# Optimization experiments

Hardware: AMD Instinct MI355X
Metric: run time of the kernel (lower is better)

Reference implementation:

```python
import jax, jax.numpy as jnp
import numpy as np

B, L, D_MODEL, H, DK = 4, 1024, 1024, 16, 64
FILTER_LENGTHS = (2, 4)
FMAX = max(FILTER_LENGTHS)


def setup_inputs() -> dict:
    key = jax.random.key(0)
    ks = jax.random.split(key, 12)
    s = 0.02
    inp = {
        "Q": jax.random.normal(ks[0], (B, L, D_MODEL), jnp.float32),
        "K": jax.random.normal(ks[1], (B, L, D_MODEL), jnp.float32),
        "V": jax.random.normal(ks[2], (B, L, D_MODEL), jnp.float32),
        "attn_mask": jnp.zeros((1,), jnp.bool_),
        "WQ": jax.random.normal(ks[3], (D_MODEL, H * DK), jnp.float32) * s,
        "bQ": jnp.zeros((H * DK,), jnp.float32),
        "WK": jax.random.normal(ks[4], (D_MODEL, H * DK), jnp.float32) * s,
        "bK": jnp.zeros((H * DK,), jnp.float32),
        "WV": jax.random.normal(ks[5], (D_MODEL, H * DK), jnp.float32) * s,
        "bV": jnp.zeros((H * DK,), jnp.float32),
        "Wfc": jax.random.normal(ks[6], (H * DK, D_MODEL), jnp.float32) * s,
        "bfc": jnp.zeros((D_MODEL,), jnp.float32),
        "conv_q": jax.random.normal(ks[7], (H * DK, H * DK, FMAX), jnp.float32) * s,
        "conv_k": jax.random.normal(ks[8], (H * DK, H * DK, FMAX), jnp.float32) * s,
        "w": jax.random.normal(ks[9], (len(FILTER_LENGTHS),), jnp.float32),
    }
    return inp


def _get_conv(x4, conv, w):
    # x4: (b, h, l, d_k) -> ACAT.get_conv with torch-identical raw reshapes
    b, h, l, d_k = x4.shape
    sig = x4.reshape(b, h * d_k, l)            # raw row-major reshape (as torch)
    pad = jnp.pad(sig, ((0, 0), (0, 0), (FMAX // 2, FMAX // 2)))
    idx = jnp.arange(l)[:, None] + jnp.arange(FMAX)[None, :]   # (l, FMAX) unfold windows
    seq = pad[:, :, idx]                        # (b, d, l, FMAX)
    f_s = jnp.array(FILTER_LENGTHS, dtype=sig.dtype)
    w_f = f_s * w                               # einsum('f,f->f')
    ind = jnp.argmax(w_f)
    flen = jnp.array(FILTER_LENGTHS)[ind]
    mask = (jnp.arange(FMAX) < flen).astype(sig.dtype)
    seq = seq * mask                            # zero out trailing taps
    out = jnp.einsum('bdlf,dof->blo', seq, conv)  # o = h*d_k
    return out.reshape(b, h, l, d_k)            # raw reshape as in torch code


def reference(Q, K, V, attn_mask, WQ, bQ, WK, bK, WV, bV, Wfc, bfc, conv_q, conv_k, w):
    b, l, _ = Q.shape
    q = (Q @ WQ + bQ).reshape(b, l, H, DK).transpose(0, 2, 1, 3)  # (b,h,l,dk)
    k = (K @ WK + bK).reshape(b, l, H, DK).transpose(0, 2, 1, 3)
    v = (V @ WV + bV).reshape(b, l, H, DK).transpose(0, 2, 1, 3)
    q = _get_conv(q, conv_q, w) + q
    k = _get_conv(k, conv_k, w) + k
    scores = jnp.einsum('bhqd,bhkd->bhqk', q, k) / np.sqrt(DK).astype(np.float32)
    attn = jax.nn.softmax(scores, axis=-1)
    ctx = jnp.einsum('bhqk,bhkd->bhqd', attn, v)
    ctx = ctx.transpose(0, 2, 1, 3).reshape(b, l, H * DK)
    out = ctx @ Wfc + bfc
    return out
```

## Files before the change

### kernel.cpp

```cpp
#include <hip/hip_runtime.h>
#include <hip/hip_bf16.h>

typedef _Float16 f16;
typedef _Float16 f16x2 __attribute__((ext_vector_type(2)));
typedef _Float16 f16x4 __attribute__((ext_vector_type(4)));
typedef _Float16 f16x8 __attribute__((ext_vector_type(8)));
typedef float f32x4 __attribute__((ext_vector_type(4)));

__device__ __forceinline__ f16x2 pkrtz(float a, float b) {
    auto r = __builtin_amdgcn_cvt_pkrtz(a, b);
    f16x2 o; o[0] = (f16)r[0]; o[1] = (f16)r[1];
    return o;
}

#define XT_ROWS 1027
#define XT_BSTRIDE (XT_ROWS * 1024)

__device__ __forceinline__ void gload16(const f16* g, f16* l) {
    __builtin_amdgcn_global_load_lds(
        (const __attribute__((address_space(1))) void*)g,
        (__attribute__((address_space(3))) void*)l, 16, 0, 0);
}

__device__ __forceinline__ void stage_tile(const f16* src, int ld, f16* lds)
{
    const int tid = threadIdx.x;
    const int w512 = (tid >> 6) << 9;
    #pragma unroll
    for (int q = 0; q < 4; ++q) {
        const int s = q * 256 + tid;
        const int row = s >> 3;
        const int col = ((s & 7) ^ (row & 7)) << 3;
        gload16(src + row * ld + col, lds + (q << 11) + w512);
    }
}

__device__ __forceinline__ void stage64(const f16* src, int ld, f16* lds)
{
    const int tid = threadIdx.x;
    const int w512 = (tid >> 6) << 9;
    #pragma unroll
    for (int q = 0; q < 2; ++q) {
        const int s = q * 256 + tid;
        const int row = s >> 3;
        const int col = ((s & 7) ^ (row & 7)) << 3;
        gload16(src + row * ld + col, lds + (q << 11) + w512);
    }
}

template <int CONV>
__device__ __forceinline__ void gemm_core64(
    const f16* __restrict__ A, int lda, int m0,
    const f16* __restrict__ Bt, int ldb, int K,
    f16* Alds, f16* Blds, f32x4 acc[4][4])
{
    const int tid = threadIdx.x;
    const int lid = tid & 63;
    const int wv  = tid >> 6;
    const int wm  = (wv >> 1) * 64;
    const int wn  = (wv & 1) * 64;
    const int g   = lid >> 4;
    const int r15 = lid & 15;

    stage_tile(A + m0 * lda, lda, Alds);
    stage_tile(Bt, ldb, Blds);
    asm volatile("s_waitcnt vmcnt(0)" ::: "memory");
    __builtin_amdgcn_s_barrier();

    for (int k0 = 0; k0 < K; k0 += 64) {
        f16x8 af[2][4], bf[2][4];
        #pragma unroll
        for (int kc = 0; kc < 2; ++kc) {
            #pragma unroll
            for (int mi = 0; mi < 4; ++mi) {
                const int row = wm + mi * 16 + r15;
                af[kc][mi] = *(const f16x8*)(Alds + row * 64 +
                                             (((kc * 4 + g) ^ (row & 7)) << 3));
            }
            #pragma unroll
            for (int nj = 0; nj < 4; ++nj) {
                const int row = wn + nj * 16 + r15;
                bf[kc][nj] = *(const f16x8*)(Blds + row * 64 +
                                             (((kc * 4 + g) ^ (row & 7)) << 3));
            }
        }
        asm volatile("s_waitcnt lgkmcnt(0)" ::: "memory");
        __builtin_amdgcn_sched_barrier(0);
        __builtin_amdgcn_s_barrier();
        const int k1 = k0 + 64;
        if (k1 < K) {
            const f16* Asrc;
            if (CONV) Asrc = A + (m0 + (k1 >> 10)) * lda + (k1 & 1023);
            else      Asrc = A + m0 * lda + k1;
            stage_tile(Asrc, lda, Alds);
            stage_tile(Bt + k1, ldb, Blds);
        }
        __builtin_amdgcn_sched_barrier(0);
        #pragma unroll
        for (int kc = 0; kc < 2; ++kc)
            #pragma unroll
            for (int mi = 0; mi < 4; ++mi)
                #pragma unroll
                for (int nj = 0; nj < 4; ++nj)
                    acc[mi][nj] = __builtin_amdgcn_mfma_f32_16x16x32_f16(
                        af[kc][mi], bf[kc][nj], acc[mi][nj], 0, 0, 0);
        __builtin_amdgcn_sched_barrier(0);
        asm volatile("s_waitcnt vmcnt(0)" ::: "memory");
        __builtin_amdgcn_s_barrier();
    }
}

__global__ __launch_bounds__(256) void k_cvt_all(
    const float* __restrict__ Q, const float* __restrict__ K,
    const float* __restrict__ V, f16* __restrict__ Qh,
    f16* __restrict__ Kh, f16* __restrict__ Vh)
{
    const int bid = blockIdx.x;
    const int which = bid >> 12;
    const int i = (bid & 4095) * 256 + threadIdx.x;
    const float* in = which == 0 ? Q : which == 1 ? K : V;
    f16* out = which == 0 ? Qh : which == 1 ? Kh : Vh;
    float4 v = ((const float4*)in)[i];
    f16x4 o;
    o[0] = (f16)v.x; o[1] = (f16)v.y; o[2] = (f16)v.z; o[3] = (f16)v.w;
    ((f16x4*)out)[i] = o;
}

__global__ __launch_bounds__(256) void k_wtrans(
    const float* __restrict__ WQ, const float* __restrict__ WK,
    const float* __restrict__ WV, const float* __restrict__ Wfc,
    f16* __restrict__ WQt, f16* __restrict__ WKt,
    f16* __restrict__ WVt, f16* __restrict__ WFt)
{
    const int z = blockIdx.z;
    const float* in = z == 0 ? WQ : z == 1 ? WK : z == 2 ? WV : Wfc;
    f16* out = z == 0 ? WQt : z == 1 ? WKt : z == 2 ? WVt : WFt;
    __shared__ float tile[32][33];
    int c0 = blockIdx.x * 32, r0 = blockIdx.y * 32;
    int tx = threadIdx.x, ty = threadIdx.y;
    #pragma unroll
    for (int i = ty; i < 32; i += 8)
        tile[i][tx] = in[(size_t)(r0 + i) * 1024 + c0 + tx];
    __syncthreads();
    #pragma unroll
    for (int i = ty; i < 32; i += 8)
        out[(size_t)(c0 + i) * 1024 + r0 + tx] = (f16)tile[tx][i];
}

__global__ __launch_bounds__(256) void k_ctrans(
    const float* __restrict__ convq, const float* __restrict__ convk,
    f16* __restrict__ CTq, f16* __restrict__ CTk)
{
    const float* in = blockIdx.z ? convk : convq;
    f16* out = blockIdx.z ? CTk : CTq;
    __shared__ float tile[32][33];
    int c0 = blockIdx.x * 32, r0 = blockIdx.y * 32;
    int tx = threadIdx.x, ty = threadIdx.y;
    #pragma unroll
    for (int i = ty; i < 32; i += 8)
        tile[i][tx] = in[(size_t)(r0 + i) * 4096 + c0 + tx];
    __syncthreads();
    #pragma unroll
    for (int i = ty; i < 32; i += 8)
        out[(size_t)(c0 + i) * 1024 + r0 + tx] = (f16)tile[tx][i];
}

__global__ __launch_bounds__(256) void k_transpose_pad(
    const f16* __restrict__ qx4, const f16* __restrict__ kx4,
    f16* __restrict__ XtQ, f16* __restrict__ XtK)
{
    int z = blockIdx.z, b = z & 3, ten = z >> 2;
    const f16* in = (ten ? kx4 : qx4) + (size_t)b * 1048576;
    f16* out = (ten ? XtK : XtQ) + (size_t)b * XT_BSTRIDE;
    __shared__ f16 tile[32][33];
    int c0 = blockIdx.x * 32;
    int tp0 = blockIdx.y * 32;
    int tx = threadIdx.x, ty = threadIdx.y;
    #pragma unroll
    for (int i = ty; i < 32; i += 8) {
        int t = tp0 + tx - 2;
        tile[i][tx] = (t >= 0 && t < 1024) ? in[(c0 + i) * 1024 + t] : (f16)0.f;
    }
    __syncthreads();
    #pragma unroll
    for (int i = ty; i < 32; i += 8) {
        int tp = tp0 + i;
        if (tp < XT_ROWS) out[tp * 1024 + c0 + tx] = tile[tx][i];
    }
}

__global__ __launch_bounds__(256) void k_gemm_proj(
    const f16* __restrict__ Qh, const f16* __restrict__ Kh, const f16* __restrict__ Vh,
    const f16* __restrict__ WQt, const f16* __restrict__ WKt, const f16* __restrict__ WVt,
    const float* __restrict__ bQ, const float* __restrict__ bK, const float* __restrict__ bV,
    f16* __restrict__ qx4, f16* __restrict__ kx4, f16* __restrict__ vT)
{
    __shared__ __align__(16) f16 Alds[128 * 64];
    __shared__ __align__(16) f16 Blds[128 * 64];
    const int nid = blockIdx.x + blockIdx.y * 8 + blockIdx.z * 256;
    const int wgid = (nid & 7) * 96 + (nid >> 3);
    const int xw = wgid & 7, yw = (wgid >> 3) & 31, z = wgid >> 8;
    const f16* A  = z == 0 ? Qh : z == 1 ? Kh : Vh;
    const f16* Bt = z == 0 ? WQt : z == 1 ? WKt : WVt;
    const float* bias = z == 0 ? bQ : z == 1 ? bK : bV;
    f16* dst = z == 0 ? qx4 : z == 1 ? kx4 : vT;
    const int m0 = yw * 128, n0 = xw * 128;
    f32x4 acc[4][4] = {};
    gemm_core64<0>(A, 1024, m0, Bt + n0 * 1024, 1024, 1024, Alds, Blds, acc);

    const int tid = threadIdx.x, lid = tid & 63, wv = tid >> 6;
    const int wm = (wv >> 1) * 64, wn = (wv & 1) * 64, g = lid >> 4, r15 = lid & 15;
    #pragma unroll
    for (int nj = 0; nj < 4; ++nj) {
        const int col = n0 + wn + nj * 16 + r15;
        const float bv = bias[col];
        const int h = col >> 6, d = col & 63;
        #pragma unroll
        for (int mi = 0; mi < 4; ++mi)
            #pragma unroll
            for (int j = 0; j < 4; ++j) {
                const int row = m0 + wm + mi * 16 + g * 4 + j;
                const int b = row >> 10, l = row & 1023;
                const float v = acc[mi][nj][j] + bv;
                const int off = b * 1048576 + h * 65536 +
                                (z == 2 ? (d * 1024 + l) : (l * 64 + d));
                dst[off] = (f16)v;
            }
    }
}

__global__ __launch_bounds__(256) void k_gemm_conv(
    const f16* __restrict__ XtQ, const f16* __restrict__ XtK,
    const f16* __restrict__ CTq, const f16* __restrict__ CTk,
    f16* __restrict__ qx4, f16* __restrict__ kx4,
    const float* __restrict__ wvec)
{
    __shared__ __align__(16) f16 Alds[128 * 64];
    __shared__ __align__(16) f16 Blds[128 * 64];
    const int nid = blockIdx.x + blockIdx.y * 8 + blockIdx.z * 64;
    const int z = nid & 7;
    const int inner = nid >> 3;
    const int yw = inner & 7;
    const int xw = inner >> 3;
    const int b = z & 3, ten = z >> 2;
    const f16* Xt = (ten ? XtK : XtQ) + (size_t)b * XT_BSTRIDE;
    const f16* CT = ten ? CTk : CTq;
    f16* dst = (ten ? kx4 : qx4) + (size_t)b * 1048576;

    const int flen = (2.f * wvec[0] >= 4.f * wvec[1]) ? 2 : 4;
    const int K = flen << 10;

    const int m0 = yw * 128, n0 = xw * 128;
    f32x4 acc[4][4] = {};
    gemm_core64<1>(Xt, 1024, m0, CT + n0 * 4096, 4096, K, Alds, Blds, acc);

    const int tid = threadIdx.x, lid = tid & 63, wv = tid >> 6;
    const int wm = (wv >> 1) * 64, wn = (wv & 1) * 64, g = lid >> 4, r15 = lid & 15;
    #pragma unroll
    for (int nj = 0; nj < 4; ++nj) {
        const int col = n0 + wn + nj * 16 + r15;
        #pragma unroll
        for (int mi = 0; mi < 4; ++mi)
            #pragma unroll
            for (int j = 0; j < 4; ++j) {
                const int row = m0 + wm + mi * 16 + g * 4 + j;
                const int i = row * 1024 + col;
                dst[i] = (f16)(acc[mi][nj][j] + (float)dst[i]);
            }
    }
}

__device__ __forceinline__ void attn_tile(
    const f16* KL, const f16* VL,
    const f16* Kn, const f16* Vn, f16* KLn, f16* VLn, bool doStage,
    const f16x8 qf[2][2], f32x4 o[2][4], f32x4 lsum[2], int g, int r15)
{
    f16x8 kf[4][2];
    #pragma unroll
    for (int nj = 0; nj < 4; ++nj)
        #pragma unroll
        for (int kc = 0; kc < 2; ++kc) {
            const int row = nj * 16 + r15;
            kf[nj][kc] = *(const f16x8*)(KL + row * 64 +
                                         (((kc * 4 + g) ^ (row & 7)) << 3));
        }
    f16x4 vlo[4][2], vhi[4][2];
    #pragma unroll
    for (int db = 0; db < 4; ++db)
        #pragma unroll
        for (int ch = 0; ch < 2; ++ch) {
            const int row = db * 16 + r15;
            const int c1 = ch * 4 + (g >> 1);
            const int c2 = c1 + 2;
            const int sub = (g & 1) * 4;
            vlo[db][ch] = *(const f16x4*)(VL + row * 64 +
                                          ((c1 ^ (row & 7)) << 3) + sub);
            vhi[db][ch] = *(const f16x4*)(VL + row * 64 +
                                          ((c2 ^ (row & 7)) << 3) + sub);
        }
    asm volatile("s_waitcnt lgkmcnt(0)" ::: "memory");
    __builtin_amdgcn_sched_barrier(0);
    __builtin_amdgcn_s_barrier();
    if (doStage) {
        stage64(Kn, 64, KLn);
        stage64(Vn, 1024, VLn);
    }
    __builtin_amdgcn_sched_barrier(0);
    f32x4 sacc[2][4] = {};
    #pragma unroll
    for (int nj = 0; nj < 4; ++nj)
        #pragma unroll
        for (int kc = 0; kc < 2; ++kc) {
            sacc[0][nj] = __builtin_amdgcn_mfma_f32_16x16x32_f16(
                kf[nj][kc], qf[0][kc], sacc[0][nj], 0, 0, 0);
            sacc[1][nj] = __builtin_amdgcn_mfma_f32_16x16x32_f16(
                kf[nj][kc], qf[1][kc], sacc[1][nj], 0, 0, 0);
        }
    #pragma unroll
    for (int qh = 0; qh < 2; ++qh) {
        f32x4 pe[4];
        #pragma unroll
        for (int nj = 0; nj < 4; ++nj) {
            #pragma unroll
            for (int j = 0; j < 4; ++j)
                pe[nj][j] = __expf(sacc[qh][nj][j] - 2.0f);
            lsum[qh] += pe[nj];
        }
        f16x8 pb[2];
        #pragma unroll
        for (int ch = 0; ch < 2; ++ch) {
            union { f16x2 h2[4]; f16x8 v8; } u;
            u.h2[0] = pkrtz(pe[2 * ch][0], pe[2 * ch][1]);
            u.h2[1] = pkrtz(pe[2 * ch][2], pe[2 * ch][3]);
            u.h2[2] = pkrtz(pe[2 * ch + 1][0], pe[2 * ch + 1][1]);
            u.h2[3] = pkrtz(pe[2 * ch + 1][2], pe[2 * ch + 1][3]);
            pb[ch] = u.v8;
        }
        #pragma unroll
        for (int db = 0; db < 4; ++db)
            #pragma unroll
            for (int ch = 0; ch < 2; ++ch) {
                union { f16x4 h4[2]; f16x8 v8; } w;
                w.h4[0] = vlo[db][ch];
                w.h4[1] = vhi[db][ch];
                o[qh][db] = __builtin_amdgcn_mfma_f32_16x16x32_f16(
                    w.v8, pb[ch], o[qh][db], 0, 0, 0);
            }
    }
    __builtin_amdgcn_sched_barrier(0);
    asm volatile("s_waitcnt vmcnt(0)" ::: "memory");
    __builtin_amdgcn_s_barrier();
}

__global__ __launch_bounds__(256) void k_attn(
    const f16* __restrict__ qn, const f16* __restrict__ kn,
    const f16* __restrict__ vT, f16* __restrict__ ctx)
{
    __shared__ __align__(16) f16 lds[4][4096];
    const int bh = blockIdx.x, b = bh >> 4, h = bh & 15;
    const f16* Qp = qn + (size_t)b * 1048576 + h * 65536;
    const f16* Kp = kn + (size_t)b * 1048576 + h * 65536;
    const f16* Vp = vT + (size_t)b * 1048576 + h * 65536;
    const int tid = threadIdx.x, lid = tid & 63, wv = tid >> 6;
    const int g = lid >> 4, r15 = lid & 15;
    const int q0 = blockIdx.y * 128 + wv * 32;

    f16x8 qf[2][2];
    #pragma unroll
    for (int qh = 0; qh < 2; ++qh)
        #pragma unroll
        for (int kc = 0; kc < 2; ++kc) {
            f16x8 t = *(const f16x8*)(Qp + (q0 + qh * 16 + r15) * 64 + kc * 32 + g * 8);
            #pragma unroll
            for (int e = 0; e < 8; ++e) t[e] = t[e] * (f16)0.125f;
            qf[qh][kc] = t;
        }

    f32x4 o[2][4] = {};
    f32x4 lsum[2] = {};

    stage64(Kp, 64, lds[0]);
    stage64(Vp, 1024, lds[1]);
    asm volatile("s_waitcnt vmcnt(0)" ::: "memory");
    __builtin_amdgcn_s_barrier();

    for (int tt = 0; tt < 8; ++tt) {
        const int t1 = 2 * tt + 1;
        attn_tile(lds[0], lds[1], Kp + t1 * 4096, Vp + t1 * 64,
                  lds[2], lds[3], true, qf, o, lsum, g, r15);
        attn_tile(lds[2], lds[3], Kp + (t1 + 1) * 4096, Vp + (t1 + 1) * 64,
                  lds[0], lds[1], tt < 7, qf, o, lsum, g, r15);
    }

    float inv[2];
    #pragma unroll
    for (int qh = 0; qh < 2; ++qh) {
        float lr = lsum[qh][0] + lsum[qh][1] + lsum[qh][2] + lsum[qh][3];
        lr += __shfl_xor(lr, 16);
        lr += __shfl_xor(lr, 32);
        inv[qh] = 1.0f / lr;
    }
    f16* Olds = &lds[0][0] + wv * (32 * 72);
    #pragma unroll
    for (int qh = 0; qh < 2; ++qh)
        #pragma unroll
        for (int db = 0; db < 4; ++db) {
            const int row = qh * 16 + r15, col = db * 16 + g * 4;
            *(f16x2*)(Olds + row * 72 + col) =
                pkrtz(o[qh][db][0] * inv[qh], o[qh][db][1] * inv[qh]);
            *(f16x2*)(Olds + row * 72 + col + 2) =
                pkrtz(o[qh][db][2] * inv[qh], o[qh][db][3] * inv[qh]);
        }
    asm volatile("s_waitcnt lgkmcnt(0)" ::: "memory");
    __builtin_amdgcn_sched_barrier(0);
    #pragma unroll
    for (int p = 0; p < 4; ++p) {
        const int row = p * 8 + (lid >> 3);
        const int c8 = (lid & 7) * 8;
        f16x8 v = *(const f16x8*)(Olds + row * 72 + c8);
        *(f16x8*)(ctx + (size_t)b * 1048576 + (q0 + row) * 1024 + h * 64 + c8) = v;
    }
}

__global__ __launch_bounds__(256) void k_gemm_final(
    const f16* __restrict__ ctx, const f16* __restrict__ WFt,
    const float* __restrict__ bfc, float* __restrict__ out)
{
    __shared__ __align__(16) f16 Alds[128 * 64];
    __shared__ __align__(16) f16 Blds[128 * 64];
    const int nid = blockIdx.x + blockIdx.y * 8;
    const int wgid = (nid & 7) * 32 + (nid >> 3);
    const int xw = wgid & 7, yw = wgid >> 3;
    const int m0 = yw * 128, n0 = xw * 128;
    f32x4 acc[4][4] = {};
    gemm_core64<0>(ctx, 1024, m0, WFt + n0 * 1024, 1024, 1024, Alds, Blds, acc);

    const int tid = threadIdx.x, lid = tid & 63, wv = tid >> 6;
    const int wm = (wv >> 1) * 64, wn = (wv & 1) * 64, g = lid >> 4, r15 = lid & 15;
    #pragma unroll
    for (int nj = 0; nj < 4; ++nj) {
        const int col = n0 + wn + nj * 16 + r15;
        const float bv = bfc[col];
        #pragma unroll
        for (int mi = 0; mi < 4; ++mi)
            #pragma unroll
            for (int j = 0; j < 4; ++j) {
                const int row = m0 + wm + mi * 16 + g * 4 + j;
                out[(size_t)row * 1024 + col] = acc[mi][nj][j] + bv;
            }
    }
}

extern "C" void kernel_launch(void* const* d_in, const int* in_sizes, int n_in,
                              void* d_out, int out_size, void* d_ws, size_t ws_size,
                              hipStream_t stream)
{
    (void)in_sizes; (void)n_in; (void)out_size; (void)ws_size;
    const float* Q     = (const float*)d_in[0];
    const float* K     = (const float*)d_in[1];
    const float* V     = (const float*)d_in[2];
    const float* WQ    = (const float*)d_in[4];
    const float* bQ    = (const float*)d_in[5];
    const float* WK    = (const float*)d_in[6];
    const float* bK    = (const float*)d_in[7];
    const float* WV    = (const float*)d_in[8];
    const float* bV    = (const float*)d_in[9];
    const float* Wfc   = (const float*)d_in[10];
    const float* bfc   = (const float*)d_in[11];
    const float* convq = (const float*)d_in[12];
    const float* convk = (const float*)d_in[13];
    const float* w     = (const float*)d_in[14];

    char* ws = (char*)d_ws;
    f16* qx4   = (f16*)(ws + 0);
    f16* kx4   = (f16*)(ws + 8388608);
    f16* vT    = (f16*)(ws + 16777216);
    f16* WFt   = (f16*)(ws + 25165824);
    f16* Qh    = (f16*)(ws + 27262976);
    f16* Kh    = (f16*)(ws + 35651584);
    f16* Vh    = (f16*)(ws + 44040192);
    f16* WQt   = (f16*)(ws + 52428800);
    f16* WKt   = (f16*)(ws + 54525952);
    f16* WVt   = (f16*)(ws + 56623104);
    f16* CTq   = (f16*)(ws + 58720256);
    f16* XtQ   = (f16*)(ws + 27262976);
    f16* XtK   = (f16*)(ws + 35676160);
    f16* CTk   = (f16*)(ws + 44089344);
    f16* ctxb  = (f16*)(ws + 27262976);

    dim3 b256(256), bT(32, 8);

    k_cvt_all<<<12288, b256, 0, stream>>>(Q, K, V, Qh, Kh, Vh);
    k_wtrans<<<dim3(32, 32, 4), bT, 0, stream>>>(WQ, WK, WV, Wfc,
                                                 WQt, WKt, WVt, WFt);
    k_gemm_proj<<<dim3(8, 32, 3), b256, 0, stream>>>(Qh, Kh, Vh, WQt, WKt, WVt,
                                                     bQ, bK, bV, qx4, kx4, vT);
    k_transpose_pad<<<dim3(32, 33, 8), bT, 0, stream>>>(qx4, kx4, XtQ, XtK);
    k_ctrans<<<dim3(128, 32, 2), bT, 0, stream>>>(convq, convk, CTq, CTk);
    k_gemm_conv<<<dim3(8, 8, 8), b256, 0, stream>>>(XtQ, XtK, CTq, CTk,
                                                    qx4, kx4, w);
    k_attn<<<dim3(64, 8), b256, 0, stream>>>(qx4, kx4, vT, ctxb);
    k_gemm_final<<<dim3(8, 32), b256, 0, stream>>>(ctxb, WFt, bfc, (float*)d_out);
}
```

Before: 182.3 us.

## Double-buffer LDS tiles in shared GEMM core to prefetch two stages ahead

Replaces the single-buffer GEMM main loop with a double-buffered one. The loop now prefetches the tile two k-steps ahead and waits with a partial vmcnt, so global loads overlap more of the MFMA work. LDS use per block doubles to 64 KB, which can reduce occupancy. The vmcnt(8) count assumes each stage issues exactly 8 loads, so correctness depends on the stage_tile load count.

```diff
diff --git a/kernel.cpp b/kernel.cpp
--- a/kernel.cpp
+++ b/kernel.cpp
@@ -49,10 +49,10 @@
 }
 
 template <int CONV>
-__device__ __forceinline__ void gemm_core64(
+__device__ __forceinline__ void gemm_core_db(
     const f16* __restrict__ A, int lda, int m0,
     const f16* __restrict__ Bt, int ldb, int K,
-    f16* Alds, f16* Blds, f32x4 acc[4][4])
+    f16* Alds0, f16* Blds0, f16* Alds1, f16* Blds1, f32x4 acc[4][4])
 {
     const int tid = threadIdx.x;
     const int lid = tid & 63;
@@ -62,38 +62,47 @@
     const int g   = lid >> 4;
     const int r15 = lid & 15;
 
-    stage_tile(A + m0 * lda, lda, Alds);
-    stage_tile(Bt, ldb, Blds);
-    asm volatile("s_waitcnt vmcnt(0)" ::: "memory");
+    stage_tile(CONV ? A + m0 * lda : A + m0 * lda, lda, Alds0);
+    stage_tile(Bt, ldb, Blds0);
+    {
+        const f16* As1 = CONV ? A + m0 * lda + 64 : A + m0 * lda + 64;
+        stage_tile(As1, lda, Alds1);
+        stage_tile(Bt + 64, ldb, Blds1);
+    }
+    asm volatile("s_waitcnt vmcnt(8)" ::: "memory");
     __builtin_amdgcn_s_barrier();
 
     for (int k0 = 0; k0 < K; k0 += 64) {
+        const int cur = (k0 >> 6) & 1;
+        f16* Al = cur ? Alds1 : Alds0;
+        f16* Bl = cur ? Blds1 : Blds0;
         f16x8 af[2][4], bf[2][4];
         #pragma unroll
         for (int kc = 0; kc < 2; ++kc) {
             #pragma unroll
             for (int mi = 0; mi < 4; ++mi) {
                 const int row = wm + mi * 16 + r15;
-                af[kc][mi] = *(const f16x8*)(Alds + row * 64 +
+                af[kc][mi] = *(const f16x8*)(Al + row * 64 +
                                              (((kc * 4 + g) ^ (row & 7)) << 3));
             }
             #pragma unroll
             for (int nj = 0; nj < 4; ++nj) {
                 const int row = wn + nj * 16 + r15;
-                bf[kc][nj] = *(const f16x8*)(Blds + row * 64 +
+                bf[kc][nj] = *(const f16x8*)(Bl + row * 64 +
                                              (((kc * 4 + g) ^ (row & 7)) << 3));
             }
         }
         asm volatile("s_waitcnt lgkmcnt(0)" ::: "memory");
         __builtin_amdgcn_sched_barrier(0);
         __builtin_amdgcn_s_barrier();
-        const int k1 = k0 + 64;
-        if (k1 < K) {
+        const int k2 = k0 + 128;
+        const bool issued = k2 < K;
+        if (issued) {
             const f16* Asrc;
-            if (CONV) Asrc = A + (m0 + (k1 >> 10)) * lda + (k1 & 1023);
-            else      Asrc = A + m0 * lda + k1;
-            stage_tile(Asrc, lda, Alds);
-            stage_tile(Bt + k1, ldb, Blds);
+            if (CONV) Asrc = A + (m0 + (k2 >> 10)) * lda + (k2 & 1023);
+            else      Asrc = A + m0 * lda + k2;
+            stage_tile(Asrc, lda, Al);
+            stage_tile(Bt + k2, ldb, Bl);
         }
         __builtin_amdgcn_sched_barrier(0);
         #pragma unroll
@@ -105,8 +114,11 @@
                     acc[mi][nj] = __builtin_amdgcn_mfma_f32_16x16x32_f16(
                         af[kc][mi], bf[kc][nj], acc[mi][nj], 0, 0, 0);
         __builtin_amdgcn_sched_barrier(0);
-        asm volatile("s_waitcnt vmcnt(0)" ::: "memory");
-        __builtin_amdgcn_s_barrier();
+        if (k0 + 64 < K) {
+            if (issued) asm volatile("s_waitcnt vmcnt(8)" ::: "memory");
+            else        asm volatile("s_waitcnt vmcnt(0)" ::: "memory");
+            __builtin_amdgcn_s_barrier();
+        }
     }
 }
 
@@ -195,8 +207,8 @@
     const float* __restrict__ bQ, const float* __restrict__ bK, const float* __restrict__ bV,
     f16* __restrict__ qx4, f16* __restrict__ kx4, f16* __restrict__ vT)
 {
-    __shared__ __align__(16) f16 Alds[128 * 64];
-    __shared__ __align__(16) f16 Blds[128 * 64];
+    __shared__ __align__(16) f16 Alds[2][128 * 64];
+    __shared__ __align__(16) f16 Blds[2][128 * 64];
     const int nid = blockIdx.x + blockIdx.y * 8 + blockIdx.z * 256;
     const int wgid = (nid & 7) * 96 + (nid >> 3);
     const int xw = wgid & 7, yw = (wgid >> 3) & 31, z = wgid >> 8;
@@ -206,7 +218,8 @@
     f16* dst = z == 0 ? qx4 : z == 1 ? kx4 : vT;
     const int m0 = yw * 128, n0 = xw * 128;
     f32x4 acc[4][4] = {};
-    gemm_core64<0>(A, 1024, m0, Bt + n0 * 1024, 1024, 1024, Alds, Blds, acc);
+    gemm_core_db<0>(A, 1024, m0, Bt + n0 * 1024, 1024, 1024,
+                    Alds[0], Blds[0], Alds[1], Blds[1], acc);
 
     const int tid = threadIdx.x, lid = tid & 63, wv = tid >> 6;
     const int wm = (wv >> 1) * 64, wn = (wv & 1) * 64, g = lid >> 4, r15 = lid & 15;
@@ -235,8 +248,8 @@
     f16* __restrict__ qx4, f16* __restrict__ kx4,
     const float* __restrict__ wvec)
 {
-    __shared__ __align__(16) f16 Alds[128 * 64];
-    __shared__ __align__(16) f16 Blds[128 * 64];
+    __shared__ __align__(16) f16 Alds[2][128 * 64];
+    __shared__ __align__(16) f16 Blds[2][128 * 64];
     const int nid = blockIdx.x + blockIdx.y * 8 + blockIdx.z * 64;
     const int z = nid & 7;
     const int inner = nid >> 3;
@@ -252,7 +265,8 @@
 
     const int m0 = yw * 128, n0 = xw * 128;
     f32x4 acc[4][4] = {};
-    gemm_core64<1>(Xt, 1024, m0, CT + n0 * 4096, 4096, K, Alds, Blds, acc);
+    gemm_core_db<1>(Xt, 1024, m0, CT + n0 * 4096, 4096, K,
+                    Alds[0], Blds[0], Alds[1], Blds[1], acc);
 
     const int tid = threadIdx.x, lid = tid & 63, wv = tid >> 6;
     const int wm = (wv >> 1) * 64, wn = (wv & 1) * 64, g = lid >> 4, r15 = lid & 15;
@@ -426,14 +440,15 @@
     const f16* __restrict__ ctx, const f16* __restrict__ WFt,
     const float* __restrict__ bfc, float* __restrict__ out)
 {
-    __shared__ __align__(16) f16 Alds[128 * 64];
-    __shared__ __align__(16) f16 Blds[128 * 64];
+    __shared__ __align__(16) f16 Alds[2][128 * 64];
+    __shared__ __align__(16) f16 Blds[2][128 * 64];
     const int nid = blockIdx.x + blockIdx.y * 8;
     const int wgid = (nid & 7) * 32 + (nid >> 3);
     const int xw = wgid & 7, yw = wgid >> 3;
     const int m0 = yw * 128, n0 = xw * 128;
     f32x4 acc[4][4] = {};
-    gemm_core64<0>(ctx, 1024, m0, WFt + n0 * 1024, 1024, 1024, Alds, Blds, acc);
+    gemm_core_db<0>(ctx, 1024, m0, WFt + n0 * 1024, 1024, 1024,
+                    Alds[0], Blds[0], Alds[1], Blds[1], acc);
 
     const int tid = threadIdx.x, lid = tid & 63, wv = tid >> 6;
     const int wm = (wv >> 1) * 64, wn = (wv & 1) * 64, g = lid >> 4, r15 = lid & 15;
```

Measured after the change: 198.7 us. 1.09x slower.
